# Kernel tuning notes

Hardware: AMD Instinct MI355X
Metric: run time of the kernel (lower is better)

## Reference

```python
import jax, jax.numpy as jnp
import numpy as np

B, T, HID = 2, 512, 1024
H, D, K = 16, 64, 4          # heads, head_dim, short-conv kernel
P = H * D                    # projection_dim
E, TOPK, I, IS = 8, 2, 768, 768  # experts, top_k, expert inter, shared inter
EPS = 1e-5


def setup_inputs() -> dict:
    key = jax.random.key(0)
    ks = jax.random.split(key, 24)
    def r(i, shape, s=0.02):
        return jax.random.normal(ks[i], shape, jnp.float32) * s
    return {
        "x": jax.random.normal(ks[0], (B, T, HID), jnp.float32),
        "norm1_w": jnp.ones((HID,), jnp.float32),
        "wq": r(1, (HID, P)), "wk": r(2, (HID, P)), "wv": r(3, (HID, P)),
        "cq": r(4, (P, K), 0.5), "ck": r(5, (P, K), 0.5), "cv": r(6, (P, K), 0.5),
        "fa": r(7, (HID, D)), "fb": r(8, (D, P)), "bp": r(9, (HID, H)),
        "ga": r(10, (HID, D)), "gb": r(11, (D, P)),
        "A_log": jnp.log(jax.random.uniform(ks[12], (H, 1), jnp.float32, 1.0, 16.0)),
        "dt_bias": r(13, (H, D), 0.1),
        "onorm_w": jnp.ones((D,), jnp.float32),
        "wo": r(14, (P, HID)),
        "norm2_w": jnp.ones((HID,), jnp.float32),
        "gate_w": r(15, (HID, E)), "gate_b": r(16, (E,), 0.1),
        "wg_e": r(17, (E, HID, I)), "wu_e": r(18, (E, HID, I)), "wd_e": r(19, (E, I, HID)),
        "wg_s": r(20, (HID, IS)), "wu_s": r(21, (HID, IS)), "wd_s": r(22, (IS, HID)),
    }


def _rms(x, w, eps=EPS):
    return x * jax.lax.rsqrt(jnp.mean(x * x, axis=-1, keepdims=True) + eps) * w


def _dwconv_silu(x, w):
    # causal depthwise conv, NLC layout: out[b,t,c] = sum_k w[c,k] * x[b, t-(K-1)+k, c]
    xp = jnp.pad(x, ((0, 0), (K - 1, 0), (0, 0)))
    out = sum(w[:, k] * xp[:, k:k + x.shape[1], :] for k in range(K))
    return jax.nn.silu(out)


def _delta_attn(x, wq, wk, wv, cq, ck, cv, fa, fb, bp, ga, gb, A_log, dt_bias, onorm_w, wo):
    q = _dwconv_silu(x @ wq, cq).reshape(B, T, H, D)
    k = _dwconv_silu(x @ wk, ck).reshape(B, T, H, D)
    v = _dwconv_silu(x @ wv, cv).reshape(B, T, H, D)
    # L2-style rms normalization of q/k (no weight, eps=1e-6), then asymmetric scaling
    q = q * jax.lax.rsqrt(jnp.mean(q * q, -1, keepdims=True) + 1e-6)
    k = k * jax.lax.rsqrt(jnp.mean(k * k, -1, keepdims=True) + 1e-6)
    scale = float(D) ** -0.5
    q = (scale ** 2) * q
    k = scale * k
    # fine-grained per-channel gated decay + per-head write strength
    a = ((x @ fa) @ fb).reshape(B, T, H, D)
    g = jnp.exp(-jnp.exp(A_log)[None, None] * jax.nn.softplus(a + dt_bias))  # (B,T,H,D)
    beta = jax.nn.sigmoid(x @ bp)  # (B,T,H)

    def step(S, qkvgb):
        qt, kt, vt, gt, bt = qkvgb            # (B,H,D) each, bt (B,H)
        S = S * gt[..., None]                  # decay over key dim, S: (B,H,Dk,Dv)
        pred = jnp.einsum('bhk,bhkv->bhv', kt, S)
        S = S + jnp.einsum('bhk,bhv->bhkv', kt, (vt - pred) * bt[..., None])
        o = jnp.einsum('bhk,bhkv->bhv', qt, S)
        return S, o

    xs = tuple(jnp.moveaxis(t_, 1, 0) for t_ in (q, k, v, g, beta))
    S0 = jnp.zeros((B, H, D, D), x.dtype)
    _, o = jax.lax.scan(step, S0, xs)
    o = jnp.moveaxis(o, 0, 1)                  # (B,T,H,D)
    gate = ((x @ ga) @ gb).reshape(B, T, H, D)
    o = _rms(o, onorm_w) * jax.nn.sigmoid(gate)
    return o.reshape(B, T, P) @ wo


def _moe(x, gate_w, gate_b, wg_e, wu_e, wd_e, wg_s, wu_s, wd_s):
    n = x.reshape(-1, HID)                     # (N, HID)
    scores = jax.nn.sigmoid(n @ gate_w)        # sigmoid router
    biased = scores + gate_b                   # e_score_correction bias (selection only)
    _, inds = jax.lax.top_k(biased, TOPK)      # n_group==1 -> plain top-k
    w = jnp.take_along_axis(scores, inds, -1)  # gather ORIGINAL scores
    w = w / (w.sum(-1, keepdims=True) + 1e-20) # renormalize; routed_scaling=1.0
    N = n.shape[0]
    comb = jnp.zeros((N, E), n.dtype).at[jnp.arange(N)[:, None], inds].add(w)
    hg = jnp.einsum('nd,edi->eni', n, wg_e)
    hu = jnp.einsum('nd,edi->eni', n, wu_e)
    eo = jnp.einsum('eni,eih->enh', jax.nn.silu(hg) * hu, wd_e)
    routed = jnp.einsum('ne,enh->nh', comb, eo)
    shared = (jax.nn.silu(n @ wg_s) * (n @ wu_s)) @ wd_s
    return (routed + shared).reshape(x.shape)


def _forward(x, norm1_w, wq, wk, wv, cq, ck, cv, fa, fb, bp, ga, gb, A_log, dt_bias,
             onorm_w, wo, norm2_w, gate_w, gate_b, wg_e, wu_e, wd_e, wg_s, wu_s, wd_s):
    h = x + _delta_attn(_rms(x, norm1_w), wq, wk, wv, cq, ck, cv, fa, fb, bp, ga, gb,
                        A_log, dt_bias, onorm_w, wo)
    return h + _moe(_rms(h, norm2_w), gate_w, gate_b, wg_e, wu_e, wd_e, wg_s, wu_s, wd_s)


def reference(x, norm1_w, wq, wk, wv, cq, ck, cv, fa, fb, bp, ga, gb, A_log, dt_bias,
              onorm_w, wo, norm2_w, gate_w, gate_b, wg_e, wu_e, wd_e, wg_s, wu_s, wd_s):
    return _forward(x, norm1_w, wq, wk, wv, cq, ck, cv, fa, fb, bp, ga, gb, A_log,
                    dt_bias, onorm_w, wo, norm2_w, gate_w, gate_b, wg_e, wu_e, wd_e,
                    wg_s, wu_s, wd_s)
```

## Files before the change

kernel.cpp:

```cpp
#include <hip/hip_runtime.h>
#include <hip/hip_bf16.h>
#include <math.h>

#define Bb 2
#define Tt 512
#define HIDD 1024
#define Hh 16
#define Dd 64
#define Pp 1024
#define Kc 4
#define Ee 8
#define Ii 768
#define ISs 768
#define Ntok (Bb*Tt)
#define NASSIGN (2*Ntok)
#define NPAD 2112
#define SCH 8
#define SNCH (Tt/SCH)

typedef __attribute__((ext_vector_type(8))) short bf16x8;
typedef __attribute__((ext_vector_type(4))) float floatx4;

__device__ __forceinline__ float sigmoidf_(float x){ return 1.f/(1.f+expf(-x)); }
__device__ __forceinline__ float siluf_(float x){ return x/(1.f+expf(-x)); }
__device__ __forceinline__ float bf2f(__hip_bfloat16 b){ return __bfloat162float(b); }

__device__ __forceinline__ void async16(void* lds, const void* g) {
  __builtin_amdgcn_global_load_lds(
      (const __attribute__((address_space(1))) void*)g,
      (__attribute__((address_space(3))) void*)lds, 16, 0, 0);
}

template<int CTRL>
__device__ __forceinline__ float dpp_add(float x){
  int y = __builtin_amdgcn_update_dpp(0, __float_as_int(x), CTRL, 0xF, 0xF, true);
  return x + __int_as_float(y);
}

__device__ __forceinline__ void ds_read128(floatx4& d, const float* p){
  asm volatile("ds_read_b128 %0, %1"
    : "=v"(d)
    : "v"((const __attribute__((address_space(3))) float*)p));
}
__device__ __forceinline__ void ds_read32f(float& d, const float* p){
  asm volatile("ds_read_b32 %0, %1"
    : "=v"(d)
    : "v"((const __attribute__((address_space(3))) float*)p));
}

__global__ void rms_split_kernel(const float* __restrict__ x, const float* __restrict__ w,
                                 __hip_bfloat16* __restrict__ hi, __hip_bfloat16* __restrict__ lo,
                                 float eps) {
  int row = blockIdx.x;
  const float* xr = x + (size_t)row*HIDD;
  float s = 0.f;
  for (int i = threadIdx.x; i < HIDD; i += 256){ float v = xr[i]; s += v*v; }
  #pragma unroll
  for (int off=32; off; off>>=1) s += __shfl_down(s, off, 64);
  __shared__ float red[4];
  if ((threadIdx.x & 63)==0) red[threadIdx.x>>6] = s;
  __syncthreads();
  float tot = red[0]+red[1]+red[2]+red[3];
  float sc = rsqrtf(tot/(float)HIDD + eps);
  for (int i = threadIdx.x; i < HIDD; i += 256) {
    float v = xr[i]*sc*w[i];
    __hip_bfloat16 h = __float2bfloat16(v);
    hi[(size_t)row*HIDD+i] = h;
    lo[(size_t)row*HIDD+i] = __float2bfloat16(v - bf2f(h));
  }
}

__global__ void trans_split4_kernel(const float* __restrict__ wq, const float* __restrict__ wk,
                                    const float* __restrict__ wv, const float* __restrict__ wo,
                                    __hip_bfloat16* __restrict__ qkv_hi, __hip_bfloat16* __restrict__ qkv_lo,
                                    __hip_bfloat16* __restrict__ wo_hi, __hip_bfloat16* __restrict__ wo_lo) {
  int z = blockIdx.z;
  const float* src = (z==0)?wq:(z==1)?wk:(z==2)?wv:wo;
  __hip_bfloat16* hi = (z<3) ? qkv_hi + (size_t)z*Pp*HIDD : wo_hi;
  __hip_bfloat16* lo = (z<3) ? qkv_lo + (size_t)z*Pp*HIDD : wo_lo;
  __shared__ float tile[32][33];
  int n0 = blockIdx.x*32, k0 = blockIdx.y*32;
  int tx = threadIdx.x & 31, ty0 = threadIdx.x >> 5;
  #pragma unroll
  for (int j=0;j<4;j++){ int ty = ty0 + j*8; tile[ty][tx] = src[(size_t)(k0+ty)*1024 + n0+tx]; }
  __syncthreads();
  #pragma unroll
  for (int j=0;j<4;j++){
    int ty = ty0 + j*8;
    float v = tile[tx][ty];
    __hip_bfloat16 h = __float2bfloat16(v);
    hi[(size_t)(n0+ty)*1024 + k0+tx] = h;
    lo[(size_t)(n0+ty)*1024 + k0+tx] = __float2bfloat16(v - bf2f(h));
  }
}

__global__ void trans_kernel(const float* __restrict__ src, __hip_bfloat16* __restrict__ dst,
                             int K, int N, long sbs, long dbs) {
  src += (size_t)blockIdx.z * sbs; dst += (size_t)blockIdx.z * dbs;
  __shared__ float tile[32][33];
  int n0 = blockIdx.x*32, k0 = blockIdx.y*32;
  int tx = threadIdx.x & 31, ty0 = threadIdx.x >> 5;
  #pragma unroll
  for (int j=0;j<4;j++){ int ty = ty0 + j*8; tile[ty][tx] = src[(size_t)(k0+ty)*N + n0+tx]; }
  __syncthreads();
  #pragma unroll
  for (int j=0;j<4;j++){ int ty = ty0 + j*8; dst[(size_t)(n0+ty)*K + k0+tx] = __float2bfloat16(tile[tx][ty]); }
}

__global__ void trans_pair_kernel(const float* __restrict__ a, const float* __restrict__ b2,
                                  __hip_bfloat16* __restrict__ da, __hip_bfloat16* __restrict__ db,
                                  int K, int N) {
  const float* src = blockIdx.z ? b2 : a;
  __hip_bfloat16* dst = blockIdx.z ? db : da;
  __shared__ float tile[32][33];
  int n0 = blockIdx.x*32, k0 = blockIdx.y*32;
  int tx = threadIdx.x & 31, ty0 = threadIdx.x >> 5;
  #pragma unroll
  for (int j=0;j<4;j++){ int ty = ty0 + j*8; tile[ty][tx] = src[(size_t)(k0+ty)*N + n0+tx]; }
  __syncthreads();
  #pragma unroll
  for (int j=0;j<4;j++){ int ty = ty0 + j*8; dst[(size_t)(n0+ty)*K + k0+tx] = __float2bfloat16(tile[tx][ty]); }
}

__global__ void trans_inter_kernel(const float* __restrict__ sa, const float* __restrict__ sb2,
                                   __hip_bfloat16* __restrict__ dst, int K, int N,
                                   long sbs, long dbs) {
  int e = blockIdx.z >> 1, phase = blockIdx.z & 1;
  const float* src = (phase ? sb2 : sa) + (size_t)e*sbs;
  dst += (size_t)e*dbs;
  __shared__ float tile[32][33];
  int n0 = blockIdx.x*32, k0 = blockIdx.y*32;
  int tx = threadIdx.x & 31, ty0 = threadIdx.x >> 5;
  #pragma unroll
  for (int j=0;j<4;j++){ int ty = ty0 + j*8; tile[ty][tx] = src[(size_t)(k0+ty)*N + n0+tx]; }
  __syncthreads();
  #pragma unroll
  for (int j=0;j<4;j++){
    int ty = ty0 + j*8;
    dst[(size_t)(2*(n0+ty)+phase)*K + k0+tx] = __float2bfloat16(tile[tx][ty]);
  }
}

__device__ __forceinline__ int lds_off(int row, int slot){
  return row*128 + (((slot ^ row)&7)<<4);
}

template<int MODE, int ACC>
__global__ __launch_bounds__(256)
void gemm_k(const __hip_bfloat16* __restrict__ A, const __hip_bfloat16* __restrict__ BT,
            void* __restrict__ C, int M, int N, int K, int lda, const float* __restrict__ resid,
            const int* __restrict__ counts, const int* __restrict__ prefix,
            const int* __restrict__ ctok, const int* __restrict__ cslot,
            const float* __restrict__ cwt) {
  int Me = M;
  int moff = 0;
  if (MODE == 3 || MODE == 4 || MODE == 6) {
    int e = blockIdx.z;
    Me = counts[e]; moff = prefix[e];
    A  += (size_t)moff * lda;
    BT += (size_t)e * (size_t)N * K;
  }
  int row0 = blockIdx.y * 64;
  if (row0 >= Me) return;
  int col0 = blockIdx.x * 64;

  __shared__ __attribute__((aligned(16))) short As[64*64];
  __shared__ __attribute__((aligned(16))) short Bs[64*64];
  const int lane = threadIdx.x & 63;
  const int w    = threadIdx.x >> 6;
  const int wr = w >> 1, wc = w & 1;
  const int srow = lane >> 3;
  const int sch  = (lane & 7) ^ (srow & 7);
  const int q = lane >> 4, r16 = lane & 15;

  const __hip_bfloat16* Ag = A  + (size_t)row0 * lda;
  const __hip_bfloat16* Bg = BT + (size_t)col0 * K;

  floatx4 acc[2][2] = {};

  for (int k0 = 0; k0 < K; k0 += 64) {
    #pragma unroll
    for (int ii = 0; ii < 2; ++ii) {
      const int inst = w + ii*4;
      const int r = inst*8 + srow;
      async16((char*)As + inst*1024, Ag + (size_t)r*lda + (size_t)(k0 + sch*8));
      async16((char*)Bs + inst*1024, Bg + (size_t)r*K   + (size_t)(k0 + sch*8));
    }
    __syncthreads();
    #pragma unroll
    for (int kk = 0; kk < 2; ++kk) {
      int slot = kk*4 + q;
      bf16x8 a0 = *(const bf16x8*)((const char*)As + lds_off(wr*32 +      r16, slot));
      bf16x8 a1 = *(const bf16x8*)((const char*)As + lds_off(wr*32 + 16 + r16, slot));
      bf16x8 b0 = *(const bf16x8*)((const char*)Bs + lds_off(wc*32 +      r16, slot));
      bf16x8 b1 = *(const bf16x8*)((const char*)Bs + lds_off(wc*32 + 16 + r16, slot));
      acc[0][0] = __builtin_amdgcn_mfma_f32_16x16x32_bf16(a0, b0, acc[0][0], 0, 0, 0);
      acc[0][1] = __builtin_amdgcn_mfma_f32_16x16x32_bf16(a0, b1, acc[0][1], 0, 0, 0);
      acc[1][0] = __builtin_amdgcn_mfma_f32_16x16x32_bf16(a1, b0, acc[1][0], 0, 0, 0);
      acc[1][1] = __builtin_amdgcn_mfma_f32_16x16x32_bf16(a1, b1, acc[1][1], 0, 0, 0);
    }
    __syncthreads();
  }

  #pragma unroll
  for (int mi = 0; mi < 2; ++mi) {
    #pragma unroll
    for (int r = 0; r < 4; ++r) {
      int grow = row0 + wr*32 + mi*16 + q*4 + r;
      if (grow >= Me) continue;
      #pragma unroll
      for (int ni = 0; ni < 2; ++ni) {
        int gcol = col0 + wc*32 + ni*16 + r16;
        float v = acc[mi][ni][r];
        if (MODE == 0) {
          float* Cp = (float*)C + (size_t)grow*N + gcol;
          if (ACC) v += *Cp;
          *Cp = v;
        } else if (MODE == 2) {
          float* Cp = (float*)C + (size_t)grow*N + gcol;
          if (ACC) v += *Cp;
          *Cp = v + resid[(size_t)grow*N + gcol];
        } else if (MODE == 1) {
          ((__hip_bfloat16*)C)[(size_t)grow*N + gcol] = __float2bfloat16(v);
        } else if (MODE == 3) {
          ((__hip_bfloat16*)C)[(size_t)(moff+grow)*N + gcol] = __float2bfloat16(v);
        } else if (MODE == 4) {
          int rc = moff + grow;
          int tok = ctok[rc], sl = cslot[rc];
          ((__hip_bfloat16*)C)[((size_t)tok*2 + sl)*N + gcol] = __float2bfloat16(cwt[rc]*v);
        } else if (MODE == 5) {
          int hh2 = gcol >> 6, d2 = gcol & 63;
          float t2 = v + cwt[hh2*64 + d2];
          float sp = (t2 > 20.f) ? t2 : log1pf(expf(t2));
          ((float*)C)[(size_t)grow*N + gcol] = expf(-expf(resid[hh2]) * sp);
        } else {
          float pv = __shfl_xor(v, 1, 64);
          if ((lane & 1) == 0) {
            float rglu = siluf_(v) * pv;
            int pcol = gcol >> 1;
            size_t orow = (MODE == 6) ? (size_t)(moff + grow) : (size_t)grow;
            ((__hip_bfloat16*)C)[orow*(N/2) + pcol] = __float2bfloat16(rglu);
          }
        }
      }
    }
  }
}

template<int MODE>
__global__ __launch_bounds__(256)
void gemm3_k(const __hip_bfloat16* __restrict__ Ahi, const __hip_bfloat16* __restrict__ Alo,
             const __hip_bfloat16* __restrict__ Bhi, const __hip_bfloat16* __restrict__ Blo,
             float* __restrict__ C, int M, int N, int K, const float* __restrict__ resid) {
  int row0 = blockIdx.y * 64;
  int col0 = blockIdx.x * 64;

  __shared__ __attribute__((aligned(16))) short As[64*64];
  __shared__ __attribute__((aligned(16))) short Bs[64*64];
  const int lane = threadIdx.x & 63;
  const int w    = threadIdx.x >> 6;
  const int wr = w >> 1, wc = w & 1;
  const int srow = lane >> 3;
  const int sch  = (lane & 7) ^ (srow & 7);
  const int q = lane >> 4, r16 = lane & 15;

  floatx4 acc[2][2] = {};

  for (int p = 0; p < 3; ++p) {
    const __hip_bfloat16* Ag = ((p==2)? Alo : Ahi) + (size_t)row0 * K;
    const __hip_bfloat16* Bg = ((p==1)? Blo : Bhi) + (size_t)col0 * K;
    for (int k0 = 0; k0 < K; k0 += 64) {
      #pragma unroll
      for (int ii = 0; ii < 2; ++ii) {
        const int inst = w + ii*4;
        const int r = inst*8 + srow;
        async16((char*)As + inst*1024, Ag + (size_t)r*K + (size_t)(k0 + sch*8));
        async16((char*)Bs + inst*1024, Bg + (size_t)r*K + (size_t)(k0 + sch*8));
      }
      __syncthreads();
      #pragma unroll
      for (int kk = 0; kk < 2; ++kk) {
        int slot = kk*4 + q;
        bf16x8 a0 = *(const bf16x8*)((const char*)As + lds_off(wr*32 +      r16, slot));
        bf16x8 a1 = *(const bf16x8*)((const char*)As + lds_off(wr*32 + 16 + r16, slot));
        bf16x8 b0 = *(const bf16x8*)((const char*)Bs + lds_off(wc*32 +      r16, slot));
        bf16x8 b1 = *(const bf16x8*)((const char*)Bs + lds_off(wc*32 + 16 + r16, slot));
        acc[0][0] = __builtin_amdgcn_mfma_f32_16x16x32_bf16(a0, b0, acc[0][0], 0, 0, 0);
        acc[0][1] = __builtin_amdgcn_mfma_f32_16x16x32_bf16(a0, b1, acc[0][1], 0, 0, 0);
        acc[1][0] = __builtin_amdgcn_mfma_f32_16x16x32_bf16(a1, b0, acc[1][0], 0, 0, 0);
        acc[1][1] = __builtin_amdgcn_mfma_f32_16x16x32_bf16(a1, b1, acc[1][1], 0, 0, 0);
      }
      __syncthreads();
    }
  }

  #pragma unroll
  for (int mi = 0; mi < 2; ++mi) {
    #pragma unroll
    for (int r = 0; r < 4; ++r) {
      int grow = row0 + wr*32 + mi*16 + q*4 + r;
      #pragma unroll
      for (int ni = 0; ni < 2; ++ni) {
        int gcol = col0 + wc*32 + ni*16 + r16;
        float v = acc[mi][ni][r];
        if (MODE == 2) v += resid[(size_t)grow*N + gcol];
        C[(size_t)grow*N + gcol] = v;
      }
    }
  }
}

__global__ void conv_norm_kernel(const float* __restrict__ in,
                                 const float* __restrict__ cq, const float* __restrict__ ck,
                                 const float* __restrict__ cv,
                                 float* __restrict__ qc, float* __restrict__ kc,
                                 float* __restrict__ vc) {
  int tok = blockIdx.x;
  int mode = blockIdx.y;
  const float* w = (mode==0) ? cq : (mode==1) ? ck : cv;
  float* outp    = (mode==0) ? qc : (mode==1) ? kc : vc;
  int colOff = mode << 10;
  int t = threadIdx.x;
  int c0 = t*4;
  int tloc = tok & (Tt-1);

  float wv[4][4];
// ... 10 lines not shown
      float4 xv = *(const float4*)&in[(size_t)(tok-(Kc-1)+j)*3072 + colOff + c0];
      acc[0] += wv[0][j]*xv.x;
      acc[1] += wv[1][j]*xv.y;
      acc[2] += wv[2][j]*xv.z;
      acc[3] += wv[3][j]*xv.w;
    }
  }
  float val[4];
  #pragma unroll
  for (int i=0;i<4;i++) val[i] = siluf_(acc[i]);
  float scale = 1.f;
  if (mode < 2) {
    float ss = val[0]*val[0]+val[1]*val[1]+val[2]*val[2]+val[3]*val[3];
    ss += __shfl_xor(ss, 1, 64);
    ss += __shfl_xor(ss, 2, 64);
    ss += __shfl_xor(ss, 4, 64);
    ss += __shfl_xor(ss, 8, 64);
    scale = rsqrtf(ss/(float)Dd + 1e-6f) * ((mode==0) ? (1.f/64.f) : 0.125f);
  }
  float4 o4 = make_float4(val[0]*scale, val[1]*scale, val[2]*scale, val[3]*scale);
  *(float4*)&outp[(size_t)tok*Pp + c0] = o4;
}

__global__ void beta_kernel(const __hip_bfloat16* __restrict__ xn, const float* __restrict__ bp,
                            float* __restrict__ betab) {
  int row = blockIdx.x;
  int t = threadIdx.x;
  int n = t & 15, ch = t >> 4;
  float s = 0.f;
  for (int k = ch*64; k < ch*64+64; ++k)
    s += bf2f(xn[(size_t)row*HIDD + k]) * bp[k*16 + n];
  __shared__ float red[256];
  red[t] = s; __syncthreads();
  if (t < 16) {
    float tot = 0.f;
    #pragma unroll
    for (int c2 = 0; c2 < 16; ++c2) tot += red[c2*16 + t];
    betab[(size_t)row*16 + t] = sigmoidf_(tot);
  }
}

__global__ void moe_rms_scores_kernel(const float* __restrict__ h, const float* __restrict__ w2,
                                      const float* __restrict__ gw,
                                      __hip_bfloat16* __restrict__ hn, float* __restrict__ scores) {
  int row = blockIdx.x;
  const float* hr = h + (size_t)row*HIDD;
  float s = 0.f;
  for (int i = threadIdx.x; i < HIDD; i += 256){ float v = hr[i]; s += v*v; }
  #pragma unroll
  for (int off=32; off; off>>=1) s += __shfl_down(s, off, 64);
  __shared__ float red[4];
  if ((threadIdx.x & 63)==0) red[threadIdx.x>>6] = s;
  __syncthreads();
  float sc = rsqrtf((red[0]+red[1]+red[2]+red[3])/(float)HIDD + 1e-5f);
  float acc[Ee] = {};
  for (int i = threadIdx.x; i < HIDD; i += 256){
    float xv = hr[i]*sc*w2[i];
    hn[(size_t)row*HIDD + i] = __float2bfloat16(xv);
    #pragma unroll
    for (int e=0;e<Ee;e++) acc[e] += xv*gw[i*Ee+e];
  }
  #pragma unroll
  for (int e=0;e<Ee;e++){
    #pragma unroll
    for (int off=32; off; off>>=1) acc[e] += __shfl_down(acc[e], off, 64);
  }
  __shared__ float red2[4][Ee];
  if ((threadIdx.x & 63)==0){
// ... 129 lines not shown
__global__ void router_kernel(const float* __restrict__ logits, const float* __restrict__ gate_b,
                              int* __restrict__ counts, int* __restrict__ tok_list,
                              int* __restrict__ slot_list, float* __restrict__ wt_list) {
  int n = blockIdx.x*256 + threadIdx.x;
  if (n >= Ntok) return;
  float sc[Ee], bi[Ee];
  #pragma unroll
  for (int e=0;e<Ee;e++){ float s = sigmoidf_(logits[n*Ee+e]); sc[e]=s; bi[e]=s+gate_b[e]; }
  int i0=0;
  #pragma unroll
  for (int e=1;e<Ee;e++) if (bi[e] > bi[i0]) i0=e;
  int i1=-1;
  #pragma unroll
  for (int e=0;e<Ee;e++){ if (e==i0) continue; if (i1<0 || bi[e] > bi[i1]) i1=e; }
  float w0=sc[i0], w1=sc[i1];
  float inv = 1.f/(w0+w1+1e-20f);
  w0*=inv; w1*=inv;
  int p0 = atomicAdd(&counts[i0],1);
  tok_list[i0*Ntok+p0]=n; slot_list[i0*Ntok+p0]=0; wt_list[i0*Ntok+p0]=w0;
  int p1 = atomicAdd(&counts[i1],1);
  tok_list[i1*Ntok+p1]=n; slot_list[i1*Ntok+p1]=1; wt_list[i1*Ntok+p1]=w1;
}

__global__ void prefix_kernel(const int* __restrict__ counts, int* __restrict__ prefix) {
  if (threadIdx.x==0 && blockIdx.x==0){ int s=0; for (int e=0;e<Ee;e++){ prefix[e]=s; s+=counts[e]; } }
}

__global__ void compact_kernel(const int* __restrict__ counts, const int* __restrict__ prefix,
                               const int* __restrict__ tok_list, const int* __restrict__ slot_list,
                               const float* __restrict__ wt_list,
                               int* __restrict__ ctok, int* __restrict__ cslot, float* __restrict__ cwt) {
  int e = blockIdx.x; int c = counts[e], p = prefix[e];
  for (int i = threadIdx.x; i < c; i += 256) {
    ctok[p+i]  = tok_list[e*Ntok+i];
    cslot[p+i] = slot_list[e*Ntok+i];
    cwt[p+i]   = wt_list[e*Ntok+i];
  }
}

__global__ void gather_kernel(const __hip_bfloat16* __restrict__ hn, const int* __restrict__ ctok,
                              __hip_bfloat16* __restrict__ Ae) {
  int r = blockIdx.x;
  int t = threadIdx.x;
  ((int4*)(Ae + (size_t)r*HIDD))[t] = ((const int4*)(hn + (size_t)ctok[r]*HIDD))[t];
}

__global__ void final_kernel(const float* __restrict__ h, const __hip_bfloat16* __restrict__ routed,
                             const float* __restrict__ shr, float* __restrict__ out) {
  int idx = blockIdx.x*256 + threadIdx.x;
  if (idx >= Ntok*HIDD) return;
  int n = idx >> 10, c = idx & 1023;
  out[idx] = h[idx] + bf2f(routed[(size_t)n*2*HIDD + c]) + bf2f(routed[(size_t)n*2*HIDD + HIDD + c]) + shr[idx];
}

extern "C" void kernel_launch(void* const* d_in, const int* in_sizes, int n_in,
                              void* d_out, int out_size, void* d_ws, size_t ws_size,
                              hipStream_t stream) {
  (void)in_sizes; (void)n_in; (void)out_size; (void)ws_size;
  const float* x        = (const float*)d_in[0];
  const float* norm1_w  = (const float*)d_in[1];
  const float* wq       = (const float*)d_in[2];
  const float* wk       = (const float*)d_in[3];
  const float* wv       = (const float*)d_in[4];
  const float* cq       = (const float*)d_in[5];
  const float* ck       = (const float*)d_in[6];
  const float* cv       = (const float*)d_in[7];
  const float* fa       = (const float*)d_in[8];
  const float* fb       = (const float*)d_in[9];
  const float* bp       = (const float*)d_in[10];
  const float* ga       = (const float*)d_in[11];
  const float* gb       = (const float*)d_in[12];
  const float* A_log    = (const float*)d_in[13];
  const float* dt_bias  = (const float*)d_in[14];
  const float* onorm_w  = (const float*)d_in[15];
  const float* wo       = (const float*)d_in[16];
// ... 16 lines not shown
  };
  float* hbuf = (float*)alloc((size_t)Ntok*HIDD*4);
  size_t uStart = (off + 255) & ~(size_t)255;

  off = uStart;
  __hip_bfloat16* xn      = (__hip_bfloat16*)alloc((size_t)Ntok*HIDD*2);
  __hip_bfloat16* xn_lo   = (__hip_bfloat16*)alloc((size_t)Ntok*HIDD*2);
  __hip_bfloat16* wqkv_t  = (__hip_bfloat16*)alloc((size_t)3*Pp*HIDD*2);
  __hip_bfloat16* wqkv_lo = (__hip_bfloat16*)alloc((size_t)3*Pp*HIDD*2);
  float*          qkvlin  = (float*)alloc((size_t)Ntok*3*Pp*4);
  float*          qc      = (float*)alloc((size_t)Ntok*Pp*4);
  float*          kc      = (float*)alloc((size_t)Ntok*Pp*4);
  float*          vc      = (float*)alloc((size_t)Ntok*Pp*4);
  float*          gbuf    = (float*)alloc((size_t)Ntok*Pp*4);
  float*          gatebuf = (float*)alloc((size_t)Ntok*Pp*4);
  float*          obuf    = (float*)alloc((size_t)Ntok*Pp*4);
  __hip_bfloat16* atmp12  = (__hip_bfloat16*)alloc((size_t)Ntok*2*Dd*2);
  float*          betab   = (float*)alloc((size_t)Ntok*Hh*4);
  __hip_bfloat16* obuf_hi = (__hip_bfloat16*)alloc((size_t)Ntok*Pp*2);
  __hip_bfloat16* obuf_lo = (__hip_bfloat16*)alloc((size_t)Ntok*Pp*2);
  __hip_bfloat16* wo_t    = (__hip_bfloat16*)alloc((size_t)HIDD*Pp*2);
  __hip_bfloat16* wo_lo   = (__hip_bfloat16*)alloc((size_t)HIDD*Pp*2);
  __hip_bfloat16* fg_t    = (__hip_bfloat16*)alloc((size_t)2*Dd*HIDD*2);
  __hip_bfloat16* fb_t    = (__hip_bfloat16*)alloc((size_t)Pp*Dd*2);
  __hip_bfloat16* gb_t    = (__hip_bfloat16*)alloc((size_t)Pp*Dd*2);

  off = uStart;
  __hip_bfloat16* hn      = (__hip_bfloat16*)alloc((size_t)Ntok*HIDD*2);
  float*          scores  = (float*)alloc((size_t)Ntok*Ee*4);
  int*            counts  = (int*)alloc(64);
  int*            prefix  = (int*)alloc(64);
  int*            tok_list  = (int*)alloc((size_t)Ee*Ntok*4);
  int*            slot_list = (int*)alloc((size_t)Ee*Ntok*4);
  float*          wt_list   = (float*)alloc((size_t)Ee*Ntok*4);
  int*            ctok    = (int*)alloc((size_t)NPAD*4);
  int*            cslot   = (int*)alloc((size_t)NPAD*4);
  float*          cwt     = (float*)alloc((size_t)NPAD*4);
  __hip_bfloat16* egu_t   = (__hip_bfloat16*)alloc((size_t)Ee*2*Ii*HIDD*2);
  __hip_bfloat16* sgu_t   = (__hip_bfloat16*)alloc((size_t)2*ISs*HIDD*2);
  __hip_bfloat16* sd_t    = (__hip_bfloat16*)alloc((size_t)HIDD*ISs*2);
  __hip_bfloat16* act     = (__hip_bfloat16*)alloc((size_t)NPAD*Ii*2);
  __hip_bfloat16* sgb     = (__hip_bfloat16*)alloc((size_t)Ntok*ISs*2);
  __hip_bfloat16* routed  = (__hip_bfloat16*)alloc((size_t)Ntok*2*HIDD*2);
  float*          shout   = (float*)alloc((size_t)Ntok*HIDD*4);
  __hip_bfloat16* Ae      = (__hip_bfloat16*)alloc((size_t)NPAD*HIDD*2);
  __hip_bfloat16* ed_t    = (__hip_bfloat16*)alloc((size_t)Ee*HIDD*Ii*2);

  dim3 blk(256);
  #define NO5 nullptr, nullptr, nullptr, nullptr, nullptr

  rms_split_kernel<<<Ntok, blk, 0, stream>>>(x, norm1_w, xn, xn_lo, 1e-5f);
  trans_split4_kernel<<<dim3(32,32,4), blk, 0, stream>>>(wq, wk, wv, wo,
                                                         wqkv_t, wqkv_lo, wo_t, wo_lo);
  trans_pair_kernel<<<dim3(2,32,2), blk, 0, stream>>>(fa, ga, fg_t, fg_t + (size_t)Dd*HIDD, HIDD, Dd);
  trans_pair_kernel<<<dim3(32,2,2), blk, 0, stream>>>(fb, gb, fb_t, gb_t, Dd, Pp);

  gemm3_k<0><<<dim3(48,16,1), blk, 0, stream>>>(xn, xn_lo, wqkv_t, wqkv_lo, qkvlin,
                                                Ntok, 3*Pp, HIDD, nullptr);
  conv_norm_kernel<<<dim3(Ntok,3,1), blk, 0, stream>>>(qkvlin, cq, ck, cv, qc, kc, vc);
  gemm_k<1,0><<<dim3(2,16,1), blk, 0, stream>>>(xn, fg_t, atmp12, Ntok, 2*Dd, HIDD, HIDD, NO5, nullptr);
  gemm_k<5,0><<<dim3(16,16,1), blk, 0, stream>>>(atmp12, fb_t, gbuf, Ntok, Pp, Dd, 2*Dd,
                                                 A_log, nullptr, nullptr, nullptr, nullptr, dt_bias);
  gemm_k<0,0><<<dim3(16,16,1), blk, 0, stream>>>(atmp12+Dd, gb_t, gatebuf, Ntok, Pp, Dd, 2*Dd, NO5, nullptr);
  beta_kernel<<<Ntok, blk, 0, stream>>>(xn, bp, betab);
  scan_kernel<<<Bb*Hh*16, dim3(64), 0, stream>>>(qc, kc, vc, gbuf, betab, obuf);
  onorm_gate_split_kernel<<<(Ntok*Hh)/4, blk, 0, stream>>>(obuf, onorm_w, gatebuf, obuf_hi, obuf_lo);
  gemm3_k<2><<<dim3(16,16,1), blk, 0, stream>>>(obuf_hi, obuf_lo, wo_t, wo_lo, hbuf,
                                                Ntok, HIDD, Pp, x);

  moe_rms_scores_kernel<<<Ntok, blk, 0, stream>>>(hbuf, norm2_w, gate_w, hn, scores);
  hipMemsetAsync(counts, 0, Ee*sizeof(int), stream);
  router_kernel<<<(Ntok+255)/256, blk, 0, stream>>>(scores, gate_b, counts, tok_list, slot_list, wt_list);
  prefix_kernel<<<1, 64, 0, stream>>>(counts, prefix);
  compact_kernel<<<Ee, blk, 0, stream>>>(counts, prefix, tok_list, slot_list, wt_list, ctok, cslot, cwt);
  gather_kernel<<<NASSIGN, dim3(128), 0, stream>>>(hn, ctok, Ae);
  trans_inter_kernel<<<dim3(24,32,2*Ee), blk, 0, stream>>>(wg_e, wu_e, egu_t,
      HIDD, Ii, (long)HIDD*Ii, (long)2*Ii*HIDD);
  gemm_k<6,0><<<dim3(24,16,Ee), blk, 0, stream>>>(Ae, egu_t, act, Ntok, 2*Ii, HIDD, HIDD,
                                                  nullptr, counts, prefix, nullptr, nullptr, nullptr);
  trans_kernel<<<dim3(32,24,Ee), blk, 0, stream>>>(wd_e, ed_t,
      Ii, HIDD, (long)Ii*HIDD, (long)HIDD*Ii);
  gemm_k<4,0><<<dim3(16,16,Ee), blk, 0, stream>>>(act, ed_t, routed, Ntok, HIDD, Ii, Ii,
                                                  nullptr, counts, prefix, ctok, cslot, cwt);
  trans_inter_kernel<<<dim3(24,32,2), blk, 0, stream>>>(wg_s, wu_s, sgu_t, HIDD, ISs, 0, 0);
  trans_kernel<<<dim3(32,24,1), blk, 0, stream>>>(wd_s, sd_t, ISs, HIDD, 0, 0);
  gemm_k<7,0><<<dim3(24,16,1), blk, 0, stream>>>(hn, sgu_t, sgb, Ntok, 2*ISs, HIDD, HIDD, NO5, nullptr);
  gemm_k<0,0><<<dim3(16,16,1), blk, 0, stream>>>(sgb, sd_t, shout, Ntok, HIDD, ISs, ISs, NO5, nullptr);

  final_kernel<<<(Ntok*HIDD+255)/256, blk, 0, stream>>>(hbuf, routed, shout, out);
}
```

Before: 345.9 us.

## Fold shared expert into grouped MoE GEMMs, fuse beta and decay/gate GEMMs

The shared expert becomes a ninth expert covering every token, so one grouped gate/up GEMM and one grouped down GEMM handle both routed and shared paths. The separate shared GEMMs, transposes and the fp32 shared output buffer go away. The beta projection is folded into the RMS-norm kernel, and the decay and gate projections run as one GEMM over a concatenated zero-padded weight. The prefix kernel and memset are folded into other kernels, and the GEMMs gain a 128-wide N tile option. This reduces launches and memory traffic, at the cost of extra gather rows, a zero-padded K=128 GEMM and more registers per thread.

Result: faster. 335.1 us (median of 2 runs) (-3.1%).

```diff
diff --git a/kernel.cpp b/kernel.cpp
--- a/kernel.cpp
+++ b/kernel.cpp
@@ -14,7 +14,7 @@
 #define ISs 768
 #define Ntok (Bb*Tt)
 #define NASSIGN (2*Ntok)
-#define NPAD 2112
+#define NTOT (NASSIGN + Ntok)
 #define SCH 8
 #define SNCH (Tt/SCH)
 
@@ -48,9 +48,10 @@
     : "v"((const __attribute__((address_space(3))) float*)p));
 }
 
-__global__ void rms_split_kernel(const float* __restrict__ x, const float* __restrict__ w,
-                                 __hip_bfloat16* __restrict__ hi, __hip_bfloat16* __restrict__ lo,
-                                 float eps) {
+__global__ void rms_beta_split_kernel(const float* __restrict__ x, const float* __restrict__ w,
+                                      const float* __restrict__ bp,
+                                      __hip_bfloat16* __restrict__ hi, __hip_bfloat16* __restrict__ lo,
+                                      float* __restrict__ betab, float eps) {
   int row = blockIdx.x;
   const float* xr = x + (size_t)row*HIDD;
   float s = 0.f;
@@ -62,12 +63,29 @@
   __syncthreads();
   float tot = red[0]+red[1]+red[2]+red[3];
   float sc = rsqrtf(tot/(float)HIDD + eps);
+  float bacc[16] = {};
   for (int i = threadIdx.x; i < HIDD; i += 256) {
     float v = xr[i]*sc*w[i];
     __hip_bfloat16 h = __float2bfloat16(v);
     hi[(size_t)row*HIDD+i] = h;
     lo[(size_t)row*HIDD+i] = __float2bfloat16(v - bf2f(h));
-  }
+    #pragma unroll
+    for (int n=0;n<16;n++) bacc[n] += v * bp[i*16+n];
+  }
+  #pragma unroll
+  for (int n=0;n<16;n++){
+    #pragma unroll
+    for (int off=32; off; off>>=1) bacc[n] += __shfl_down(bacc[n], off, 64);
+  }
+  __shared__ float redb[4][16];
+  if ((threadIdx.x & 63)==0){
+    #pragma unroll
+    for (int n=0;n<16;n++) redb[threadIdx.x>>6][n] = bacc[n];
+  }
+  __syncthreads();
+  if (threadIdx.x < 16)
+    betab[(size_t)row*16 + threadIdx.x] =
+      sigmoidf_(redb[0][threadIdx.x]+redb[1][threadIdx.x]+redb[2][threadIdx.x]+redb[3][threadIdx.x]);
 }
 
 __global__ void trans_split4_kernel(const float* __restrict__ wq, const float* __restrict__ wk,
@@ -94,19 +112,6 @@
   }
 }
 
-__global__ void trans_kernel(const float* __restrict__ src, __hip_bfloat16* __restrict__ dst,
-                             int K, int N, long sbs, long dbs) {
-  src += (size_t)blockIdx.z * sbs; dst += (size_t)blockIdx.z * dbs;
-  __shared__ float tile[32][33];
-  int n0 = blockIdx.x*32, k0 = blockIdx.y*32;
-  int tx = threadIdx.x & 31, ty0 = threadIdx.x >> 5;
-  #pragma unroll
-  for (int j=0;j<4;j++){ int ty = ty0 + j*8; tile[ty][tx] = src[(size_t)(k0+ty)*N + n0+tx]; }
-  __syncthreads();
-  #pragma unroll
-  for (int j=0;j<4;j++){ int ty = ty0 + j*8; dst[(size_t)(n0+ty)*K + k0+tx] = __float2bfloat16(tile[tx][ty]); }
-}
-
 __global__ void trans_pair_kernel(const float* __restrict__ a, const float* __restrict__ b2,
                                   __hip_bfloat16* __restrict__ da, __hip_bfloat16* __restrict__ db,
                                   int K, int N) {
@@ -122,39 +127,75 @@
   for (int j=0;j<4;j++){ int ty = ty0 + j*8; dst[(size_t)(n0+ty)*K + k0+tx] = __float2bfloat16(tile[tx][ty]); }
 }
 
-__global__ void trans_inter_kernel(const float* __restrict__ sa, const float* __restrict__ sb2,
-                                   __hip_bfloat16* __restrict__ dst, int K, int N,
-                                   long sbs, long dbs) {
-  int e = blockIdx.z >> 1, phase = blockIdx.z & 1;
-  const float* src = (phase ? sb2 : sa) + (size_t)e*sbs;
-  dst += (size_t)e*dbs;
+__global__ void trans_fbgb_kernel(const float* __restrict__ fb, const float* __restrict__ gb,
+                                  __hip_bfloat16* __restrict__ dst) {
+  int z = blockIdx.z;
+  const float* src = z ? gb : fb;
   __shared__ float tile[32][33];
   int n0 = blockIdx.x*32, k0 = blockIdx.y*32;
   int tx = threadIdx.x & 31, ty0 = threadIdx.x >> 5;
   #pragma unroll
-  for (int j=0;j<4;j++){ int ty = ty0 + j*8; tile[ty][tx] = src[(size_t)(k0+ty)*N + n0+tx]; }
+  for (int j=0;j<4;j++){ int ty = ty0 + j*8; tile[ty][tx] = src[(size_t)(k0+ty)*Pp + n0+tx]; }
   __syncthreads();
   #pragma unroll
   for (int j=0;j<4;j++){
     int ty = ty0 + j*8;
-    dst[(size_t)(2*(n0+ty)+phase)*K + k0+tx] = __float2bfloat16(tile[tx][ty]);
-  }
+    size_t row = (size_t)(z*1024 + n0+ty);
+    dst[row*128 + (z?64:0) + k0+tx] = __float2bfloat16(tile[tx][ty]);
+    dst[row*128 + (z?0:64) + k0+tx] = __float2bfloat16(0.f);
+  }
+}
+
+__global__ void trans_inter9_kernel(const float* __restrict__ wg_e, const float* __restrict__ wu_e,
+                                    const float* __restrict__ wg_s, const float* __restrict__ wu_s,
+                                    __hip_bfloat16* __restrict__ dst) {
+  int e = blockIdx.z >> 1, phase = blockIdx.z & 1;
+  const float* src = (e < 8) ? ((phase ? wu_e : wg_e) + (size_t)e*HIDD*Ii)
+                             : (phase ? wu_s : wg_s);
+  dst += (size_t)e*(2*Ii*HIDD);
+  __shared__ float tile[32][33];
+  int n0 = blockIdx.x*32, k0 = blockIdx.y*32;
+  int tx = threadIdx.x & 31, ty0 = threadIdx.x >> 5;
+  #pragma unroll
+  for (int j=0;j<4;j++){ int ty = ty0 + j*8; tile[ty][tx] = src[(size_t)(k0+ty)*Ii + n0+tx]; }
+  __syncthreads();
+  #pragma unroll
+  for (int j=0;j<4;j++){
+    int ty = ty0 + j*8;
+    dst[(size_t)(2*(n0+ty)+phase)*HIDD + k0+tx] = __float2bfloat16(tile[tx][ty]);
+  }
+}
+
+__global__ void trans_down9_kernel(const float* __restrict__ wd_e, const float* __restrict__ wd_s,
+                                   __hip_bfloat16* __restrict__ dst) {
+  int z = blockIdx.z;
+  const float* src = (z < 8) ? wd_e + (size_t)z*Ii*HIDD : wd_s;
+  dst += (size_t)z*HIDD*Ii;
+  __shared__ float tile[32][33];
+  int n0 = blockIdx.x*32, k0 = blockIdx.y*32;
+  int tx = threadIdx.x & 31, ty0 = threadIdx.x >> 5;
+  #pragma unroll
+  for (int j=0;j<4;j++){ int ty = ty0 + j*8; tile[ty][tx] = src[(size_t)(k0+ty)*HIDD + n0+tx]; }
+  __syncthreads();
+  #pragma unroll
+  for (int j=0;j<4;j++){ int ty = ty0 + j*8; dst[(size_t)(n0+ty)*Ii + k0+tx] = __float2bfloat16(tile[tx][ty]); }
 }
 
 __device__ __forceinline__ int lds_off(int row, int slot){
   return row*128 + (((slot ^ row)&7)<<4);
 }
 
-template<int MODE, int ACC>
+template<int MODE, int ACC, int BND>
 __global__ __launch_bounds__(256)
 void gemm_k(const __hip_bfloat16* __restrict__ A, const __hip_bfloat16* __restrict__ BT,
             void* __restrict__ C, int M, int N, int K, int lda, const float* __restrict__ resid,
             const int* __restrict__ counts, const int* __restrict__ prefix,
             const int* __restrict__ ctok, const int* __restrict__ cslot,
             const float* __restrict__ cwt) {
+  constexpr int NF = BND/32;
   int Me = M;
   int moff = 0;
-  if (MODE == 3 || MODE == 4 || MODE == 6) {
+  if (MODE == 4 || MODE == 6) {
     int e = blockIdx.z;
     Me = counts[e]; moff = prefix[e];
     A  += (size_t)moff * lda;
@@ -162,10 +203,10 @@
   }
   int row0 = blockIdx.y * 64;
   if (row0 >= Me) return;
-  int col0 = blockIdx.x * 64;
+  int col0 = blockIdx.x * BND;
 
   __shared__ __attribute__((aligned(16))) short As[64*64];
-  __shared__ __attribute__((aligned(16))) short Bs[64*64];
+  __shared__ __attribute__((aligned(16))) short Bs[BND*64];
   const int lane = threadIdx.x & 63;
   const int w    = threadIdx.x >> 6;
   const int wr = w >> 1, wc = w & 1;
@@ -176,7 +217,7 @@
   const __hip_bfloat16* Ag = A  + (size_t)row0 * lda;
   const __hip_bfloat16* Bg = BT + (size_t)col0 * K;
 
-  floatx4 acc[2][2] = {};
+  floatx4 acc[2][NF] = {};
 
   for (int k0 = 0; k0 < K; k0 += 64) {
     #pragma unroll
@@ -184,7 +225,12 @@
       const int inst = w + ii*4;
       const int r = inst*8 + srow;
       async16((char*)As + inst*1024, Ag + (size_t)r*lda + (size_t)(k0 + sch*8));
-      async16((char*)Bs + inst*1024, Bg + (size_t)r*K   + (size_t)(k0 + sch*8));
+    }
+    #pragma unroll
+    for (int ii = 0; ii < BND/32; ++ii) {
+      const int inst = w + ii*4;
+      const int r = inst*8 + srow;
+      async16((char*)Bs + inst*1024, Bg + (size_t)r*K + (size_t)(k0 + sch*8));
     }
     __syncthreads();
     #pragma unroll
@@ -192,12 +238,15 @@
       int slot = kk*4 + q;
       bf16x8 a0 = *(const bf16x8*)((const char*)As + lds_off(wr*32 +      r16, slot));
       bf16x8 a1 = *(const bf16x8*)((const char*)As + lds_off(wr*32 + 16 + r16, slot));
-      bf16x8 b0 = *(const bf16x8*)((const char*)Bs + lds_off(wc*32 +      r16, slot));
-      bf16x8 b1 = *(const bf16x8*)((const char*)Bs + lds_off(wc*32 + 16 + r16, slot));
-      acc[0][0] = __builtin_amdgcn_mfma_f32_16x16x32_bf16(a0, b0, acc[0][0], 0, 0, 0);
-      acc[0][1] = __builtin_amdgcn_mfma_f32_16x16x32_bf16(a0, b1, acc[0][1], 0, 0, 0);
-      acc[1][0] = __builtin_amdgcn_mfma_f32_16x16x32_bf16(a1, b0, acc[1][0], 0, 0, 0);
-      acc[1][1] = __builtin_amdgcn_mfma_f32_16x16x32_bf16(a1, b1, acc[1][1], 0, 0, 0);
+      bf16x8 b[NF];
+      #pragma unroll
+      for (int ni=0; ni<NF; ++ni)
+        b[ni] = *(const bf16x8*)((const char*)Bs + lds_off(wc*(BND/2) + ni*16 + r16, slot));
+      #pragma unroll
+      for (int ni=0; ni<NF; ++ni){
+        acc[0][ni] = __builtin_amdgcn_mfma_f32_16x16x32_bf16(a0, b[ni], acc[0][ni], 0, 0, 0);
+        acc[1][ni] = __builtin_amdgcn_mfma_f32_16x16x32_bf16(a1, b[ni], acc[1][ni], 0, 0, 0);
+      }
     }
     __syncthreads();
   }
@@ -209,37 +258,29 @@
       int grow = row0 + wr*32 + mi*16 + q*4 + r;
       if (grow >= Me) continue;
       #pragma unroll
-      for (int ni = 0; ni < 2; ++ni) {
-        int gcol = col0 + wc*32 + ni*16 + r16;
+      for (int ni = 0; ni < NF; ++ni) {
+        int gcol = col0 + wc*(BND/2) + ni*16 + r16;
         float v = acc[mi][ni][r];
-        if (MODE == 0) {
-          float* Cp = (float*)C + (size_t)grow*N + gcol;
-          if (ACC) v += *Cp;
-          *Cp = v;
-        } else if (MODE == 2) {
-          float* Cp = (float*)C + (size_t)grow*N + gcol;
-          if (ACC) v += *Cp;
-          *Cp = v + resid[(size_t)grow*N + gcol];
-        } else if (MODE == 1) {
+        if (MODE == 1) {
           ((__hip_bfloat16*)C)[(size_t)grow*N + gcol] = __float2bfloat16(v);
-        } else if (MODE == 3) {
-          ((__hip_bfloat16*)C)[(size_t)(moff+grow)*N + gcol] = __float2bfloat16(v);
         } else if (MODE == 4) {
           int rc = moff + grow;
           int tok = ctok[rc], sl = cslot[rc];
-          ((__hip_bfloat16*)C)[((size_t)tok*2 + sl)*N + gcol] = __float2bfloat16(cwt[rc]*v);
-        } else if (MODE == 5) {
-          int hh2 = gcol >> 6, d2 = gcol & 63;
-          float t2 = v + cwt[hh2*64 + d2];
-          float sp = (t2 > 20.f) ? t2 : log1pf(expf(t2));
-          ((float*)C)[(size_t)grow*N + gcol] = expf(-expf(resid[hh2]) * sp);
-        } else {
+          ((__hip_bfloat16*)C)[((size_t)tok*3 + sl)*N + gcol] = __float2bfloat16(cwt[rc]*v);
+        } else if (MODE == 6) {
           float pv = __shfl_xor(v, 1, 64);
           if ((lane & 1) == 0) {
             float rglu = siluf_(v) * pv;
-            int pcol = gcol >> 1;
-            size_t orow = (MODE == 6) ? (size_t)(moff + grow) : (size_t)grow;
-            ((__hip_bfloat16*)C)[orow*(N/2) + pcol] = __float2bfloat16(rglu);
+            ((__hip_bfloat16*)C)[(size_t)(moff+grow)*(N/2) + (gcol>>1)] = __float2bfloat16(rglu);
+          }
+        } else if (MODE == 8) {
+          if (gcol < 1024) {
+            int hh2 = gcol >> 6, d2 = gcol & 63;
+            float t2 = v + cwt[hh2*64 + d2];
+            float sp = (t2 > 20.f) ? t2 : log1pf(expf(t2));
+            ((float*)C)[(size_t)grow*1024 + gcol] = expf(-expf(resid[hh2]) * sp);
+          } else {
+            ((float*)(size_t)ctok)[(size_t)grow*1024 + (gcol-1024)] = v;
           }
         }
       }
@@ -247,16 +288,17 @@
   }
 }
 
-template<int MODE>
+template<int MODE, int BND>
 __global__ __launch_bounds__(256)
 void gemm3_k(const __hip_bfloat16* __restrict__ Ahi, const __hip_bfloat16* __restrict__ Alo,
              const __hip_bfloat16* __restrict__ Bhi, const __hip_bfloat16* __restrict__ Blo,
              float* __restrict__ C, int M, int N, int K, const float* __restrict__ resid) {
+  constexpr int NF = BND/32;
   int row0 = blockIdx.y * 64;
-  int col0 = blockIdx.x * 64;
+  int col0 = blockIdx.x * BND;
 
   __shared__ __attribute__((aligned(16))) short As[64*64];
-  __shared__ __attribute__((aligned(16))) short Bs[64*64];
+  __shared__ __attribute__((aligned(16))) short Bs[BND*64];
   const int lane = threadIdx.x & 63;
   const int w    = threadIdx.x >> 6;
   const int wr = w >> 1, wc = w & 1;
@@ -264,7 +306,7 @@
   const int sch  = (lane & 7) ^ (srow & 7);
   const int q = lane >> 4, r16 = lane & 15;
 
-  floatx4 acc[2][2] = {};
+  floatx4 acc[2][NF] = {};
 
   for (int p = 0; p < 3; ++p) {
     const __hip_bfloat16* Ag = ((p==2)? Alo : Ahi) + (size_t)row0 * K;
@@ -275,6 +317,11 @@
         const int inst = w + ii*4;
         const int r = inst*8 + srow;
         async16((char*)As + inst*1024, Ag + (size_t)r*K + (size_t)(k0 + sch*8));
+      }
+      #pragma unroll
+      for (int ii = 0; ii < BND/32; ++ii) {
+        const int inst = w + ii*4;
+        const int r = inst*8 + srow;
         async16((char*)Bs + inst*1024, Bg + (size_t)r*K + (size_t)(k0 + sch*8));
       }
       __syncthreads();
@@ -283,12 +330,15 @@
         int slot = kk*4 + q;
         bf16x8 a0 = *(const bf16x8*)((const char*)As + lds_off(wr*32 +      r16, slot));
         bf16x8 a1 = *(const bf16x8*)((const char*)As + lds_off(wr*32 + 16 + r16, slot));
-        bf16x8 b0 = *(const bf16x8*)((const char*)Bs + lds_off(wc*32 +      r16, slot));
-        bf16x8 b1 = *(const bf16x8*)((const char*)Bs + lds_off(wc*32 + 16 + r16, slot));
-        acc[0][0] = __builtin_amdgcn_mfma_f32_16x16x32_bf16(a0, b0, acc[0][0], 0, 0, 0);
-        acc[0][1] = __builtin_amdgcn_mfma_f32_16x16x32_bf16(a0, b1, acc[0][1], 0, 0, 0);
-        acc[1][0] = __builtin_amdgcn_mfma_f32_16x16x32_bf16(a1, b0, acc[1][0], 0, 0, 0);
-        acc[1][1] = __builtin_amdgcn_mfma_f32_16x16x32_bf16(a1, b1, acc[1][1], 0, 0, 0);
+        bf16x8 b[NF];
+        #pragma unroll
+        for (int ni=0; ni<NF; ++ni)
+          b[ni] = *(const bf16x8*)((const char*)Bs + lds_off(wc*(BND/2) + ni*16 + r16, slot));
+        #pragma unroll
+        for (int ni=0; ni<NF; ++ni){
+          acc[0][ni] = __builtin_amdgcn_mfma_f32_16x16x32_bf16(a0, b[ni], acc[0][ni], 0, 0, 0);
+          acc[1][ni] = __builtin_amdgcn_mfma_f32_16x16x32_bf16(a1, b[ni], acc[1][ni], 0, 0, 0);
+        }
       }
       __syncthreads();
     }
@@ -300,8 +350,8 @@
     for (int r = 0; r < 4; ++r) {
       int grow = row0 + wr*32 + mi*16 + q*4 + r;
       #pragma unroll
-      for (int ni = 0; ni < 2; ++ni) {
-        int gcol = col0 + wc*32 + ni*16 + r16;
+      for (int ni = 0; ni < NF; ++ni) {
+        int gcol = col0 + wc*(BND/2) + ni*16 + r16;
         float v = acc[mi][ni][r];
         if (MODE == 2) v += resid[(size_t)grow*N + gcol];
         C[(size_t)grow*N + gcol] = v;
@@ -358,28 +408,12 @@
   *(float4*)&outp[(size_t)tok*Pp + c0] = o4;
 }
 
-__global__ void beta_kernel(const __hip_bfloat16* __restrict__ xn, const float* __restrict__ bp,
-                            float* __restrict__ betab) {
-  int row = blockIdx.x;
-  int t = threadIdx.x;
-  int n = t & 15, ch = t >> 4;
-  float s = 0.f;
-  for (int k = ch*64; k < ch*64+64; ++k)
-    s += bf2f(xn[(size_t)row*HIDD + k]) * bp[k*16 + n];
-  __shared__ float red[256];
-  red[t] = s; __syncthreads();
-  if (t < 16) {
-    float tot = 0.f;
-    #pragma unroll
-    for (int c2 = 0; c2 < 16; ++c2) tot += red[c2*16 + t];
-    betab[(size_t)row*16 + t] = sigmoidf_(tot);
-  }
-}
-
 __global__ void moe_rms_scores_kernel(const float* __restrict__ h, const float* __restrict__ w2,
                                       const float* __restrict__ gw,
-                                      __hip_bfloat16* __restrict__ hn, float* __restrict__ scores) {
+                                      __hip_bfloat16* __restrict__ hn, float* __restrict__ scores,
+                                      int* __restrict__ counts) {
   int row = blockIdx.x;
+  if (row == 0 && threadIdx.x < Ee) counts[threadIdx.x] = 0;
   const float* hr = h + (size_t)row*HIDD;
   float s = 0.f;
   for (int i = threadIdx.x; i < HIDD; i += 256){ float v = hr[i]; s += v*v; }
@@ -555,35 +589,48 @@
   tok_list[i1*Ntok+p1]=n; slot_list[i1*Ntok+p1]=1; wt_list[i1*Ntok+p1]=w1;
 }
 
-__global__ void prefix_kernel(const int* __restrict__ counts, int* __restrict__ prefix) {
-  if (threadIdx.x==0 && blockIdx.x==0){ int s=0; for (int e=0;e<Ee;e++){ prefix[e]=s; s+=counts[e]; } }
-}
-
-__global__ void compact_kernel(const int* __restrict__ counts, const int* __restrict__ prefix,
+__global__ void compact_kernel(const int* __restrict__ counts, int* __restrict__ prefix,
                                const int* __restrict__ tok_list, const int* __restrict__ slot_list,
                                const float* __restrict__ wt_list,
-                               int* __restrict__ ctok, int* __restrict__ cslot, float* __restrict__ cwt) {
-  int e = blockIdx.x; int c = counts[e], p = prefix[e];
+                               int* __restrict__ ctok, int* __restrict__ cslot, float* __restrict__ cwt,
+                               int* __restrict__ counts_mut) {
+  int e = blockIdx.x;
+  int pe = 0;
+  #pragma unroll
+  for (int j=0;j<Ee;j++) if (j < e) pe += counts[j];
+  if (threadIdx.x == 0) {
+    prefix[e] = pe;
+    if (e == 0) { prefix[Ee] = NASSIGN; counts_mut[Ee] = Ntok; }
+  }
+  int c = counts[e];
   for (int i = threadIdx.x; i < c; i += 256) {
-    ctok[p+i]  = tok_list[e*Ntok+i];
-    cslot[p+i] = slot_list[e*Ntok+i];
-    cwt[p+i]   = wt_list[e*Ntok+i];
-  }
-}
-
-__global__ void gather_kernel(const __hip_bfloat16* __restrict__ hn, const int* __restrict__ ctok,
+    ctok[pe+i]  = tok_list[e*Ntok+i];
+    cslot[pe+i] = slot_list[e*Ntok+i];
+    cwt[pe+i]   = wt_list[e*Ntok+i];
+  }
+}
+
+__global__ void gather_kernel(const __hip_bfloat16* __restrict__ hn, int* __restrict__ ctok,
+                              int* __restrict__ cslot, float* __restrict__ cwt,
                               __hip_bfloat16* __restrict__ Ae) {
   int r = blockIdx.x;
   int t = threadIdx.x;
-  ((int4*)(Ae + (size_t)r*HIDD))[t] = ((const int4*)(hn + (size_t)ctok[r]*HIDD))[t];
+  if (r < NASSIGN) {
+    ((int4*)(Ae + (size_t)r*HIDD))[t] = ((const int4*)(hn + (size_t)ctok[r]*HIDD))[t];
+  } else {
+    int tok = r - NASSIGN;
+    ((int4*)(Ae + (size_t)r*HIDD))[t] = ((const int4*)(hn + (size_t)tok*HIDD))[t];
+    if (t == 0) { ctok[r] = tok; cslot[r] = 2; cwt[r] = 1.f; }
+  }
 }
 
 __global__ void final_kernel(const float* __restrict__ h, const __hip_bfloat16* __restrict__ routed,
-                             const float* __restrict__ shr, float* __restrict__ out) {
+                             float* __restrict__ out) {
   int idx = blockIdx.x*256 + threadIdx.x;
   if (idx >= Ntok*HIDD) return;
   int n = idx >> 10, c = idx & 1023;
-  out[idx] = h[idx] + bf2f(routed[(size_t)n*2*HIDD + c]) + bf2f(routed[(size_t)n*2*HIDD + HIDD + c]) + shr[idx];
+  const __hip_bfloat16* rp = routed + (size_t)n*3*HIDD + c;
+  out[idx] = h[idx] + bf2f(rp[0]) + bf2f(rp[HIDD]) + bf2f(rp[2*HIDD]);
 }
 
 extern "C" void kernel_launch(void* const* d_in, const int* in_sizes, int n_in,
@@ -646,8 +693,7 @@
   __hip_bfloat16* wo_t    = (__hip_bfloat16*)alloc((size_t)HIDD*Pp*2);
   __hip_bfloat16* wo_lo   = (__hip_bfloat16*)alloc((size_t)HIDD*Pp*2);
   __hip_bfloat16* fg_t    = (__hip_bfloat16*)alloc((size_t)2*Dd*HIDD*2);
-  __hip_bfloat16* fb_t    = (__hip_bfloat16*)alloc((size_t)Pp*Dd*2);
-  __hip_bfloat16* gb_t    = (__hip_bfloat16*)alloc((size_t)Pp*Dd*2);
+  __hip_bfloat16* fbgb_t  = (__hip_bfloat16*)alloc((size_t)2048*128*2);
 
   off = uStart;
   __hip_bfloat16* hn      = (__hip_bfloat16*)alloc((size_t)Ntok*HIDD*2);
@@ -657,59 +703,47 @@
   int*            tok_list  = (int*)alloc((size_t)Ee*Ntok*4);
   int*            slot_list = (int*)alloc((size_t)Ee*Ntok*4);
   float*          wt_list   = (float*)alloc((size_t)Ee*Ntok*4);
-  int*            ctok    = (int*)alloc((size_t)NPAD*4);
-  int*            cslot   = (int*)alloc((size_t)NPAD*4);
-  float*          cwt     = (float*)alloc((size_t)NPAD*4);
-  __hip_bfloat16* egu_t   = (__hip_bfloat16*)alloc((size_t)Ee*2*Ii*HIDD*2);
-  __hip_bfloat16* sgu_t   = (__hip_bfloat16*)alloc((size_t)2*ISs*HIDD*2);
-  __hip_bfloat16* sd_t    = (__hip_bfloat16*)alloc((size_t)HIDD*ISs*2);
-  __hip_bfloat16* act     = (__hip_bfloat16*)alloc((size_t)NPAD*Ii*2);
-  __hip_bfloat16* sgb     = (__hip_bfloat16*)alloc((size_t)Ntok*ISs*2);
-  __hip_bfloat16* routed  = (__hip_bfloat16*)alloc((size_t)Ntok*2*HIDD*2);
-  float*          shout   = (float*)alloc((size_t)Ntok*HIDD*4);
-  __hip_bfloat16* Ae      = (__hip_bfloat16*)alloc((size_t)NPAD*HIDD*2);
-  __hip_bfloat16* ed_t    = (__hip_bfloat16*)alloc((size_t)Ee*HIDD*Ii*2);
+  int*            ctok    = (int*)alloc((size_t)(NTOT+64)*4);
+  int*            cslot   = (int*)alloc((size_t)(NTOT+64)*4);
+  float*          cwt     = (float*)alloc((size_t)(NTOT+64)*4);
+  __hip_bfloat16* egu_t   = (__hip_bfloat16*)alloc((size_t)9*2*Ii*HIDD*2);
+  __hip_bfloat16* act     = (__hip_bfloat16*)alloc((size_t)NTOT*Ii*2);
+  __hip_bfloat16* routed  = (__hip_bfloat16*)alloc((size_t)Ntok*3*HIDD*2);
+  __hip_bfloat16* Ae      = (__hip_bfloat16*)alloc((size_t)NTOT*HIDD*2);
+  __hip_bfloat16* ed_t    = (__hip_bfloat16*)alloc((size_t)9*HIDD*Ii*2);
 
   dim3 blk(256);
   #define NO5 nullptr, nullptr, nullptr, nullptr, nullptr
 
-  rms_split_kernel<<<Ntok, blk, 0, stream>>>(x, norm1_w, xn, xn_lo, 1e-5f);
+  rms_beta_split_kernel<<<Ntok, blk, 0, stream>>>(x, norm1_w, bp, xn, xn_lo, betab, 1e-5f);
   trans_split4_kernel<<<dim3(32,32,4), blk, 0, stream>>>(wq, wk, wv, wo,
                                                          wqkv_t, wqkv_lo, wo_t, wo_lo);
   trans_pair_kernel<<<dim3(2,32,2), blk, 0, stream>>>(fa, ga, fg_t, fg_t + (size_t)Dd*HIDD, HIDD, Dd);
-  trans_pair_kernel<<<dim3(32,2,2), blk, 0, stream>>>(fb, gb, fb_t, gb_t, Dd, Pp);
-
-  gemm3_k<0><<<dim3(48,16,1), blk, 0, stream>>>(xn, xn_lo, wqkv_t, wqkv_lo, qkvlin,
-                                                Ntok, 3*Pp, HIDD, nullptr);
+  trans_fbgb_kernel<<<dim3(32,2,2), blk, 0, stream>>>(fb, gb, fbgb_t);
+
+  gemm3_k<0,128><<<dim3(24,16,1), blk, 0, stream>>>(xn, xn_lo, wqkv_t, wqkv_lo, qkvlin,
+                                                    Ntok, 3*Pp, HIDD, nullptr);
   conv_norm_kernel<<<dim3(Ntok,3,1), blk, 0, stream>>>(qkvlin, cq, ck, cv, qc, kc, vc);
-  gemm_k<1,0><<<dim3(2,16,1), blk, 0, stream>>>(xn, fg_t, atmp12, Ntok, 2*Dd, HIDD, HIDD, NO5, nullptr);
-  gemm_k<5,0><<<dim3(16,16,1), blk, 0, stream>>>(atmp12, fb_t, gbuf, Ntok, Pp, Dd, 2*Dd,
-                                                 A_log, nullptr, nullptr, nullptr, nullptr, dt_bias);
-  gemm_k<0,0><<<dim3(16,16,1), blk, 0, stream>>>(atmp12+Dd, gb_t, gatebuf, Ntok, Pp, Dd, 2*Dd, NO5, nullptr);
-  beta_kernel<<<Ntok, blk, 0, stream>>>(xn, bp, betab);
+  gemm_k<1,0,64><<<dim3(2,16,1), blk, 0, stream>>>(xn, fg_t, atmp12, Ntok, 2*Dd, HIDD, HIDD, NO5, nullptr);
+  gemm_k<8,0,128><<<dim3(16,16,1), blk, 0, stream>>>(atmp12, fbgb_t, gbuf, Ntok, 2048, 128, 2*Dd,
+                                                     A_log, nullptr, nullptr,
+                                                     (const int*)gatebuf, nullptr, dt_bias);
   scan_kernel<<<Bb*Hh*16, dim3(64), 0, stream>>>(qc, kc, vc, gbuf, betab, obuf);
   onorm_gate_split_kernel<<<(Ntok*Hh)/4, blk, 0, stream>>>(obuf, onorm_w, gatebuf, obuf_hi, obuf_lo);
-  gemm3_k<2><<<dim3(16,16,1), blk, 0, stream>>>(obuf_hi, obuf_lo, wo_t, wo_lo, hbuf,
-                                                Ntok, HIDD, Pp, x);
-
-  moe_rms_scores_kernel<<<Ntok, blk, 0, stream>>>(hbuf, norm2_w, gate_w, hn, scores);
-  hipMemsetAsync(counts, 0, Ee*sizeof(int), stream);
+  gemm3_k<2,64><<<dim3(16,16,1), blk, 0, stream>>>(obuf_hi, obuf_lo, wo_t, wo_lo, hbuf,
+                                                   Ntok, HIDD, Pp, x);
+
+  moe_rms_scores_kernel<<<Ntok, blk, 0, stream>>>(hbuf, norm2_w, gate_w, hn, scores, counts);
   router_kernel<<<(Ntok+255)/256, blk, 0, stream>>>(scores, gate_b, counts, tok_list, slot_list, wt_list);
-  prefix_kernel<<<1, 64, 0, stream>>>(counts, prefix);
-  compact_kernel<<<Ee, blk, 0, stream>>>(counts, prefix, tok_list, slot_list, wt_list, ctok, cslot, cwt);
-  gather_kernel<<<NASSIGN, dim3(128), 0, stream>>>(hn, ctok, Ae);
-  trans_inter_kernel<<<dim3(24,32,2*Ee), blk, 0, stream>>>(wg_e, wu_e, egu_t,
-      HIDD, Ii, (long)HIDD*Ii, (long)2*Ii*HIDD);
-  gemm_k<6,0><<<dim3(24,16,Ee), blk, 0, stream>>>(Ae, egu_t, act, Ntok, 2*Ii, HIDD, HIDD,
-                                                  nullptr, counts, prefix, nullptr, nullptr, nullptr);
-  trans_kernel<<<dim3(32,24,Ee), blk, 0, stream>>>(wd_e, ed_t,
-      Ii, HIDD, (long)Ii*HIDD, (long)HIDD*Ii);
-  gemm_k<4,0><<<dim3(16,16,Ee), blk, 0, stream>>>(act, ed_t, routed, Ntok, HIDD, Ii, Ii,
-                                                  nullptr, counts, prefix, ctok, cslot, cwt);
-  trans_inter_kernel<<<dim3(24,32,2), blk, 0, stream>>>(wg_s, wu_s, sgu_t, HIDD, ISs, 0, 0);
-  trans_kernel<<<dim3(32,24,1), blk, 0, stream>>>(wd_s, sd_t, ISs, HIDD, 0, 0);
-  gemm_k<7,0><<<dim3(24,16,1), blk, 0, stream>>>(hn, sgu_t, sgb, Ntok, 2*ISs, HIDD, HIDD, NO5, nullptr);
-  gemm_k<0,0><<<dim3(16,16,1), blk, 0, stream>>>(sgb, sd_t, shout, Ntok, HIDD, ISs, ISs, NO5, nullptr);
-
-  final_kernel<<<(Ntok*HIDD+255)/256, blk, 0, stream>>>(hbuf, routed, shout, out);
-}
+  compact_kernel<<<Ee, blk, 0, stream>>>(counts, prefix, tok_list, slot_list, wt_list,
+                                         ctok, cslot, cwt, counts);
+  gather_kernel<<<NTOT, dim3(128), 0, stream>>>(hn, ctok, cslot, cwt, Ae);
+  trans_inter9_kernel<<<dim3(24,32,18), blk, 0, stream>>>(wg_e, wu_e, wg_s, wu_s, egu_t);
+  gemm_k<6,0,128><<<dim3(12,16,9), blk, 0, stream>>>(Ae, egu_t, act, Ntok, 2*Ii, HIDD, HIDD,
+                                                     nullptr, counts, prefix, nullptr, nullptr, nullptr);
+  trans_down9_kernel<<<dim3(32,24,9), blk, 0, stream>>>(wd_e, wd_s, ed_t);
+  gemm_k<4,0,128><<<dim3(8,16,9), blk, 0, stream>>>(act, ed_t, routed, Ntok, HIDD, Ii, Ii,
+                                                    nullptr, counts, prefix, ctok, cslot, cwt);
+
+  final_kernel<<<(Ntok*HIDD+255)/256, blk, 0, stream>>>(hbuf, routed, out);
+}
```
